# Optimization experiments

Measured on AMD Instinct MI355X. Metric: run time of the kernel, lower is better.

Reference implementation:

```python
import jax, jax.numpy as jnp
import numpy as np

N, M, D = 8192, 8192, 64


def setup_inputs() -> dict:
    key = jax.random.key(0)
    k1, k2 = jax.random.split(key)
    return {
        "x": jax.random.normal(k1, (N, D), dtype=jnp.float32),
        "y": jax.random.normal(k2, (M, D), dtype=jnp.float32),
        "log_lengthscale": jnp.zeros((D,), dtype=jnp.float32),
        "log_outputscale": jnp.zeros((1,), dtype=jnp.float32),
    }


def reference(x, y, log_lengthscale, log_outputscale):
    # ARD RBF: k(x,y) = outputscale * exp(-0.5 * sum_d ((x_d - y_d)/l_d)^2)
    lengthscale = jnp.exp(log_lengthscale)          # [D]
    outputscale = jnp.exp(log_outputscale)          # [1]
    xs = x / lengthscale                            # [N, D]
    ys = y / lengthscale                            # [M, D]
    # ||xs - ys||^2 = ||xs||^2 + ||ys||^2 - 2 xs.ys^T  (GEMM rewrite, same math)
    x2 = jnp.sum(xs * xs, axis=-1)                  # [N]
    y2 = jnp.sum(ys * ys, axis=-1)                  # [M]
    cross = jnp.einsum("nd,md->nm", xs, ys)         # [N, M]
    sq_dist = jnp.maximum(x2[:, None] + y2[None, :] - 2.0 * cross, 0.0)
    return outputscale * jnp.exp(-0.5 * sq_dist)    # [N, M]
```

## Files before the change

kernel.cpp:

```cpp
#include <hip/hip_runtime.h>
#include <hip/hip_bf16.h>

#define NROWS 8192
#define MCOLS 8192
#define DDIM  64

typedef __attribute__((ext_vector_type(8))) short bf16x8;
typedef __attribute__((ext_vector_type(4))) float f32x4;
typedef __attribute__((ext_vector_type(2))) unsigned int u32x2;
typedef __attribute__((ext_vector_type(4))) unsigned int u32x4;

#define WS_NEED (4ull * 1024 * 1024 + 64 * 1024)

__global__ __launch_bounds__(256)
void pack_kernel(const float* __restrict__ x, const float* __restrict__ y,
                 const float* __restrict__ log_l, unsigned char* __restrict__ ws)
{
    const int t = threadIdx.x, lane = t & 63, wid = t >> 6;
    const int sub = lane & 15, lg = lane >> 4;
    const int gb  = blockIdx.x;
    const int isY = gb >> 7;
    const int rb  = ((gb & 127) << 2) | wid;

    const float* __restrict__ src = isY ? y : x;
    bf16x8* __restrict__ Ph = reinterpret_cast<bf16x8*>(ws + (isY ? (2u << 20) : 0u));
    bf16x8* __restrict__ Pl = reinterpret_cast<bf16x8*>(ws + (isY ? (3u << 20) : (1u << 20)));
    float*  __restrict__ nrm = reinterpret_cast<float*>(ws + (4u << 20) + (isY ? (32u << 10) : 0u));

    const int row = rb * 16 + sub;
    float psum = 0.0f;
    #pragma unroll
    for (int kk = 0; kk < 2; ++kk) {
        const int k0 = kk * 32 + lg * 8;
        f32x4 v0 = *reinterpret_cast<const f32x4*>(&src[(size_t)row * DDIM + k0]);
        f32x4 v1 = *reinterpret_cast<const f32x4*>(&src[(size_t)row * DDIM + k0 + 4]);
        f32x4 g0 = *reinterpret_cast<const f32x4*>(&log_l[k0]);
        f32x4 g1 = *reinterpret_cast<const f32x4*>(&log_l[k0 + 4]);
        float s[8];
        #pragma unroll
        for (int j = 0; j < 4; ++j) s[j]     = v0[j] * __expf(-g0[j]);
        #pragma unroll
        for (int j = 0; j < 4; ++j) s[4 + j] = v1[j] * __expf(-g1[j]);
        unsigned int hp[4], lp[4];
        #pragma unroll
        for (int p = 0; p < 4; ++p) {
            float a = s[2 * p], b = s[2 * p + 1];
            psum += a * a + b * b;
            unsigned int ua = __float_as_uint(a), ub = __float_as_uint(b);
            float la = a - __uint_as_float(ua & 0xFFFF0000u);
            float lb = b - __uint_as_float(ub & 0xFFFF0000u);
            hp[p] = (ua >> 16) | (ub & 0xFFFF0000u);
            lp[p] = ((__float_as_uint(la) + 0x8000u) >> 16) |
                    ((__float_as_uint(lb) + 0x8000u) & 0xFFFF0000u);
        }
        const int fi = (rb * 2 + kk) * 64 + lane;
        *reinterpret_cast<u32x4*>(&Ph[fi]) = u32x4{hp[0], hp[1], hp[2], hp[3]};
        *reinterpret_cast<u32x4*>(&Pl[fi]) = u32x4{lp[0], lp[1], lp[2], lp[3]};
    }
    psum += __shfl_xor(psum, 16);
    psum += __shfl_xor(psum, 32);
    if (lg == 0) nrm[row] = psum;
}

__global__ __launch_bounds__(256, 4)
void ard_rbf_main(const unsigned char* __restrict__ ws,
                  const float* __restrict__ log_os, float* __restrict__ out)
{
    const int t = threadIdx.x, lane = t & 63, wid = t >> 6;
    const int sub = lane & 15, lg = lane >> 4;
    const int bx = blockIdx.x;
    const int by = blockIdx.y;
    const int wr = wid >> 1, wc = wid & 1;

    const bf16x8* __restrict__ Xh = reinterpret_cast<const bf16x8*>(ws);
    const bf16x8* __restrict__ Xl = reinterpret_cast<const bf16x8*>(ws + (1u << 20));
    const bf16x8* __restrict__ Yh = reinterpret_cast<const bf16x8*>(ws + (2u << 20));
    const bf16x8* __restrict__ Yl = reinterpret_cast<const bf16x8*>(ws + (3u << 20));
    const float*  __restrict__ x2 = reinterpret_cast<const float*>(ws + (4u << 20));
    const float*  __restrict__ y2 = reinterpret_cast<const float*>(ws + (4u << 20) + (32u << 10));

    const int row0 = by * 128 + wr * 64;
    const int col0 = bx * 64 + wc * 32;
    const int rbA = row0 >> 4, rbB = col0 >> 4;

    f32x4 acc[4][2] = {};
    #pragma unroll
    for (int kk = 0; kk < 2; ++kk) {
        bf16x8 ah[4], al[4];
        #pragma unroll
        for (int m = 0; m < 4; ++m) {
            const int fi = ((rbA + m) * 2 + kk) * 64 + lane;
            ah[m] = Xh[fi];
            al[m] = Xl[fi];
        }
        #pragma unroll
        for (int n = 0; n < 2; ++n) {
            const int fj = ((rbB + n) * 2 + kk) * 64 + lane;
            bf16x8 bh = Yh[fj];
            bf16x8 bl = Yl[fj];
            #pragma unroll
            for (int m = 0; m < 4; ++m) {
                acc[m][n] = __builtin_amdgcn_mfma_f32_16x16x32_bf16(ah[m], bh, acc[m][n], 0, 0, 0);
                acc[m][n] = __builtin_amdgcn_mfma_f32_16x16x32_bf16(al[m], bh, acc[m][n], 0, 0, 0);
                acc[m][n] = __builtin_amdgcn_mfma_f32_16x16x32_bf16(ah[m], bl, acc[m][n], 0, 0, 0);
            }
        }
    }

    const float lnos = log_os[0];
    float y2v[2];
    #pragma unroll
    for (int n = 0; n < 2; ++n) y2v[n] = y2[col0 + n * 16 + sub];

    #pragma unroll
    for (int m = 0; m < 4; ++m) {
        const int rbase = row0 + m * 16 + lg * 4;
        float x2v[4];
        #pragma unroll
        for (int j = 0; j < 4; ++j) x2v[j] = x2[rbase + j];
        #pragma unroll
        for (int n = 0; n < 2; ++n) {
            const size_t g0 = (size_t)rbase * MCOLS + (size_t)(col0 + n * 16 + sub);
            #pragma unroll
            for (int j = 0; j < 4; ++j) {
                float sq = fmaxf(x2v[j] + y2v[n] - 2.0f * acc[m][n][j], 0.0f);
                out[g0 + (size_t)j * MCOLS] = __expf(fmaf(-0.5f, sq, lnos));
            }
        }
    }
}

__global__ __launch_bounds__(512, 4)
void ard_rbf_fallback(const float* __restrict__ x, const float* __restrict__ y,
                      const float* __restrict__ log_l, const float* __restrict__ log_os,
                      float* __restrict__ out)
{
    __shared__ unsigned short Ah[128][DDIM + 8], Al[128][DDIM + 8];
    __shared__ unsigned short Bh[128][DDIM + 8], Bl[128][DDIM + 8];
    __shared__ float x2s[128], y2s[128];
    __shared__ float invl[DDIM];

    const int t = threadIdx.x;
    const int bx = blockIdx.x, by = blockIdx.y;
    const int lane = t & 63, sub = lane & 15, lg = lane >> 4;

    if (t < DDIM) invl[t] = __expf(-log_l[t]);
    __syncthreads();

    #pragma unroll
    for (int ab = 0; ab < 2; ++ab) {
        const float* __restrict__ src = ab ? y : x;
        unsigned short (*Hh)[DDIM + 8] = ab ? Bh : Ah;
        unsigned short (*Hl)[DDIM + 8] = ab ? Bl : Al;
        float* nrm = ab ? y2s : x2s;
        const int tb = (ab ? bx : by) * 128;
        #pragma unroll
        for (int i = 0; i < 4; ++i) {
            const int f = i * 512 + t;
            const int row = f >> 4;
            const int c4 = (f & 15) * 4;
            f32x4 v = *reinterpret_cast<const f32x4*>(&src[(size_t)(tb + row) * DDIM + c4]);
            f32x4 il = *reinterpret_cast<const f32x4*>(&invl[c4]);
            float s0 = v[0] * il[0], s1 = v[1] * il[1], s2 = v[2] * il[2], s3 = v[3] * il[3];
            float psum = s0 * s0 + s1 * s1 + s2 * s2 + s3 * s3;
            unsigned int u0 = __float_as_uint(s0), u1 = __float_as_uint(s1);
            unsigned int u2 = __float_as_uint(s2), u3 = __float_as_uint(s3);
            float l0 = s0 - __uint_as_float(u0 & 0xFFFF0000u);
            float l1 = s1 - __uint_as_float(u1 & 0xFFFF0000u);
            float l2 = s2 - __uint_as_float(u2 & 0xFFFF0000u);
            float l3 = s3 - __uint_as_float(u3 & 0xFFFF0000u);
            unsigned int hp0 = (u0 >> 16) | (u1 & 0xFFFF0000u);
            unsigned int hp1 = (u2 >> 16) | (u3 & 0xFFFF0000u);
            unsigned int lp0 = ((__float_as_uint(l0) + 0x8000u) >> 16) | ((__float_as_uint(l1) + 0x8000u) & 0xFFFF0000u);
            unsigned int lp1 = ((__float_as_uint(l2) + 0x8000u) >> 16) | ((__float_as_uint(l3) + 0x8000u) & 0xFFFF0000u);
            psum += __shfl_xor(psum, 1);
            psum += __shfl_xor(psum, 2);
            psum += __shfl_xor(psum, 4);
            psum += __shfl_xor(psum, 8);
            *reinterpret_cast<u32x2*>(&Hh[row][c4]) = u32x2{hp0, hp1};
            *reinterpret_cast<u32x2*>(&Hl[row][c4]) = u32x2{lp0, lp1};
            if (sub == 0) nrm[row] = psum;
        }
    }
    __syncthreads();

    const int wid = t >> 6;
    const int wr = wid >> 2, wc = wid & 3;
    f32x4 acc[4][2] = {};
    #pragma unroll
    for (int kk = 0; kk < 2; ++kk) {
        const int kb = kk * 32 + lg * 8;
        bf16x8 ah[4], al[4];
        #pragma unroll
        for (int m = 0; m < 4; ++m) {
            const int r = wr * 64 + m * 16 + sub;
            ah[m] = *reinterpret_cast<const bf16x8*>(&Ah[r][kb]);
            al[m] = *reinterpret_cast<const bf16x8*>(&Al[r][kb]);
        }
        #pragma unroll
        for (int n = 0; n < 2; ++n) {
            const int c = wc * 32 + n * 16 + sub;
            bf16x8 bh = *reinterpret_cast<const bf16x8*>(&Bh[c][kb]);
            bf16x8 bl = *reinterpret_cast<const bf16x8*>(&Bl[c][kb]);
            #pragma unroll
            for (int m = 0; m < 4; ++m) {
                acc[m][n] = __builtin_amdgcn_mfma_f32_16x16x32_bf16(ah[m], bh, acc[m][n], 0, 0, 0);
                acc[m][n] = __builtin_amdgcn_mfma_f32_16x16x32_bf16(al[m], bh, acc[m][n], 0, 0, 0);
                acc[m][n] = __builtin_amdgcn_mfma_f32_16x16x32_bf16(ah[m], bl, acc[m][n], 0, 0, 0);
            }
        }
    }
    const float lnos = log_os[0];
    #pragma unroll
    for (int m = 0; m < 4; ++m) {
        const int rl0 = wr * 64 + m * 16 + lg * 4;
        #pragma unroll
        for (int n = 0; n < 2; ++n) {
            const int cl = wc * 32 + n * 16 + sub;
            const float yy2 = y2s[cl];
            const size_t g0 = (size_t)(by * 128 + rl0) * MCOLS + (size_t)(bx * 128 + cl);
            #pragma unroll
            for (int j = 0; j < 4; ++j) {
                float sq = fmaxf(x2s[rl0 + j] + yy2 - 2.0f * acc[m][n][j], 0.0f);
                out[g0 + (size_t)j * MCOLS] = __expf(fmaf(-0.5f, sq, lnos));
            }
        }
    }
}

extern "C" void kernel_launch(void* const* d_in, const int* in_sizes, int n_in,
                              void* d_out, int out_size, void* d_ws, size_t ws_size,
                              hipStream_t stream) {
    const float* x      = (const float*)d_in[0];
    const float* y      = (const float*)d_in[1];
    const float* log_l  = (const float*)d_in[2];
    const float* log_os = (const float*)d_in[3];
    float* out = (float*)d_out;

    if (ws_size >= WS_NEED) {
        pack_kernel<<<256, 256, 0, stream>>>(x, y, log_l, (unsigned char*)d_ws);
        ard_rbf_main<<<dim3(128, 64), 256, 0, stream>>>((const unsigned char*)d_ws, log_os, out);
    } else {
        ard_rbf_fallback<<<dim3(64, 64), 512, 0, stream>>>(x, y, log_l, log_os, out);
    }
}
```

Baseline: 61.06 us.

## Swap MFMA operands for row-contiguous vector stores and swizzle blocks across XCDs

Swaps the MFMA A/B operands so each lane holds four consecutive output columns of one row. That allows 16-byte nontemporal vector stores instead of scalar strided stores. The grid becomes 1D with a block-index swizzle that maps consecutive blocks to different XCD groups, aiming at better L2 locality. The y2 norms are now loaded as float4. The goal is to cut store-transaction overhead on the 256MB output write, which is the dominant cost.

Result: slower. 83.10 us (+36.1%).

```diff
diff --git a/kernel.cpp b/kernel.cpp
--- a/kernel.cpp
+++ b/kernel.cpp
@@ -68,9 +68,13 @@
 {
     const int t = threadIdx.x, lane = t & 63, wid = t >> 6;
     const int sub = lane & 15, lg = lane >> 4;
-    const int bx = blockIdx.x;
-    const int by = blockIdx.y;
-    const int wr = wid >> 1, wc = wid & 1;
+
+    const int bid = (int)blockIdx.x;
+    const int swz = (bid & 7) * 1024 + (bid >> 3);
+    const int by  = swz >> 7;
+    const int bx  = swz & 127;
+    const int wr  = wid >> 1;
+    const int wc  = wid & 1;
 
     const bf16x8* __restrict__ Xh = reinterpret_cast<const bf16x8*>(ws);
     const bf16x8* __restrict__ Xl = reinterpret_cast<const bf16x8*>(ws + (1u << 20));
@@ -79,53 +83,59 @@
     const float*  __restrict__ x2 = reinterpret_cast<const float*>(ws + (4u << 20));
     const float*  __restrict__ y2 = reinterpret_cast<const float*>(ws + (4u << 20) + (32u << 10));
 
-    const int row0 = by * 128 + wr * 64;
-    const int col0 = bx * 64 + wc * 32;
-    const int rbA = row0 >> 4, rbB = col0 >> 4;
+    const int xrb = by * 8 + wr * 4;
+    const int yrb = bx * 4 + wc * 2;
 
     f32x4 acc[4][2] = {};
     #pragma unroll
     for (int kk = 0; kk < 2; ++kk) {
-        bf16x8 ah[4], al[4];
+        bf16x8 yh[2], yl[2], xh[4], xl[4];
+        #pragma unroll
+        for (int n = 0; n < 2; ++n) {
+            const int fj = ((yrb + n) * 2 + kk) * 64 + lane;
+            yh[n] = Yh[fj];
+            yl[n] = Yl[fj];
+        }
         #pragma unroll
         for (int m = 0; m < 4; ++m) {
-            const int fi = ((rbA + m) * 2 + kk) * 64 + lane;
-            ah[m] = Xh[fi];
-            al[m] = Xl[fi];
-        }
-        #pragma unroll
-        for (int n = 0; n < 2; ++n) {
-            const int fj = ((rbB + n) * 2 + kk) * 64 + lane;
-            bf16x8 bh = Yh[fj];
-            bf16x8 bl = Yl[fj];
-            #pragma unroll
-            for (int m = 0; m < 4; ++m) {
-                acc[m][n] = __builtin_amdgcn_mfma_f32_16x16x32_bf16(ah[m], bh, acc[m][n], 0, 0, 0);
-                acc[m][n] = __builtin_amdgcn_mfma_f32_16x16x32_bf16(al[m], bh, acc[m][n], 0, 0, 0);
-                acc[m][n] = __builtin_amdgcn_mfma_f32_16x16x32_bf16(ah[m], bl, acc[m][n], 0, 0, 0);
-            }
-        }
+            const int fi = ((xrb + m) * 2 + kk) * 64 + lane;
+            xh[m] = Xh[fi];
+            xl[m] = Xl[fi];
+        }
+        #pragma unroll
+        for (int m = 0; m < 4; ++m)
+            #pragma unroll
+            for (int n = 0; n < 2; ++n) {
+                acc[m][n] = __builtin_amdgcn_mfma_f32_16x16x32_bf16(yh[n], xh[m], acc[m][n], 0, 0, 0);
+                acc[m][n] = __builtin_amdgcn_mfma_f32_16x16x32_bf16(yl[n], xh[m], acc[m][n], 0, 0, 0);
+                acc[m][n] = __builtin_amdgcn_mfma_f32_16x16x32_bf16(yh[n], xl[m], acc[m][n], 0, 0, 0);
+            }
     }
 
     const float lnos = log_os[0];
-    float y2v[2];
-    #pragma unroll
-    for (int n = 0; n < 2; ++n) y2v[n] = y2[col0 + n * 16 + sub];
+    const int xbase = by * 128 + wr * 64;
+    const int ybase = bx * 64 + wc * 32;
+
+    f32x4 y2q[2];
+    #pragma unroll
+    for (int n = 0; n < 2; ++n)
+        y2q[n] = *reinterpret_cast<const f32x4*>(&y2[ybase + n * 16 + lg * 4]);
 
     #pragma unroll
     for (int m = 0; m < 4; ++m) {
-        const int rbase = row0 + m * 16 + lg * 4;
-        float x2v[4];
-        #pragma unroll
-        for (int j = 0; j < 4; ++j) x2v[j] = x2[rbase + j];
-        #pragma unroll
-        for (int n = 0; n < 2; ++n) {
-            const size_t g0 = (size_t)rbase * MCOLS + (size_t)(col0 + n * 16 + sub);
+        const int xrow = xbase + m * 16 + sub;
+        const float xs = x2[xrow];
+        float* rowp = out + (size_t)xrow * MCOLS;
+        #pragma unroll
+        for (int n = 0; n < 2; ++n) {
+            const int ycol = ybase + n * 16 + lg * 4;
+            f32x4 v;
             #pragma unroll
             for (int j = 0; j < 4; ++j) {
-                float sq = fmaxf(x2v[j] + y2v[n] - 2.0f * acc[m][n][j], 0.0f);
-                out[g0 + (size_t)j * MCOLS] = __expf(fmaf(-0.5f, sq, lnos));
-            }
+                float sq = fmaxf(xs + y2q[n][j] - 2.0f * acc[m][n][j], 0.0f);
+                v[j] = __expf(fmaf(-0.5f, sq, lnos));
+            }
+            __builtin_nontemporal_store(v, reinterpret_cast<f32x4*>(rowp + ycol));
         }
     }
 }
@@ -239,7 +249,7 @@
 
     if (ws_size >= WS_NEED) {
         pack_kernel<<<256, 256, 0, stream>>>(x, y, log_l, (unsigned char*)d_ws);
-        ard_rbf_main<<<dim3(128, 64), 256, 0, stream>>>((const unsigned char*)d_ws, log_os, out);
+        ard_rbf_main<<<8192, 256, 0, stream>>>((const unsigned char*)d_ws, log_os, out);
     } else {
         ard_rbf_fallback<<<dim3(64, 64), 512, 0, stream>>>(x, y, log_l, log_os, out);
     }
```

## Stage MFMA tiles through LDS for 16-byte coalesced output stores

Applied to the files above, without the earlier changes.

Swaps the MFMA operand order so the accumulators come out transposed. Each wave now owns 32 rows by 64 columns, writes its tile to a padded LDS buffer, and reads it back so every lane stores a contiguous float4 of output. Before, each lane wrote scalar floats spread across rows. The goal is fewer, wider global writes for an output-bandwidth-bound kernel (256MB written). The cost is LDS use and an extra shared-memory round trip per tile, which may lower occupancy.

Measured after the change: 63.17 us. 3.5% more time.

```diff
diff --git a/kernel.cpp b/kernel.cpp
--- a/kernel.cpp
+++ b/kernel.cpp
@@ -66,11 +66,12 @@
 void ard_rbf_main(const unsigned char* __restrict__ ws,
                   const float* __restrict__ log_os, float* __restrict__ out)
 {
+    __shared__ float lds[4][32][68];
+
     const int t = threadIdx.x, lane = t & 63, wid = t >> 6;
     const int sub = lane & 15, lg = lane >> 4;
     const int bx = blockIdx.x;
     const int by = blockIdx.y;
-    const int wr = wid >> 1, wc = wid & 1;
 
     const bf16x8* __restrict__ Xh = reinterpret_cast<const bf16x8*>(ws);
     const bf16x8* __restrict__ Xl = reinterpret_cast<const bf16x8*>(ws + (1u << 20));
@@ -79,54 +80,58 @@
     const float*  __restrict__ x2 = reinterpret_cast<const float*>(ws + (4u << 20));
     const float*  __restrict__ y2 = reinterpret_cast<const float*>(ws + (4u << 20) + (32u << 10));
 
-    const int row0 = by * 128 + wr * 64;
-    const int col0 = bx * 64 + wc * 32;
-    const int rbA = row0 >> 4, rbB = col0 >> 4;
-
-    f32x4 acc[4][2] = {};
+    const int xrb = by * 8 + wid * 2;
+    const int yrb = bx * 4;
+
+    f32x4 acc[2][4] = {};
     #pragma unroll
     for (int kk = 0; kk < 2; ++kk) {
-        bf16x8 ah[4], al[4];
-        #pragma unroll
-        for (int m = 0; m < 4; ++m) {
-            const int fi = ((rbA + m) * 2 + kk) * 64 + lane;
-            ah[m] = Xh[fi];
-            al[m] = Xl[fi];
-        }
-        #pragma unroll
-        for (int n = 0; n < 2; ++n) {
-            const int fj = ((rbB + n) * 2 + kk) * 64 + lane;
-            bf16x8 bh = Yh[fj];
-            bf16x8 bl = Yl[fj];
+        bf16x8 xh[2], xl[2], yh[4], yl[4];
+        #pragma unroll
+        for (int a = 0; a < 2; ++a) {
+            const int fi = ((xrb + a) * 2 + kk) * 64 + lane;
+            xh[a] = Xh[fi];
+            xl[a] = Xl[fi];
+        }
+        #pragma unroll
+        for (int b = 0; b < 4; ++b) {
+            const int fj = ((yrb + b) * 2 + kk) * 64 + lane;
+            yh[b] = Yh[fj];
+            yl[b] = Yl[fj];
+        }
+        #pragma unroll
+        for (int a = 0; a < 2; ++a)
             #pragma unroll
-            for (int m = 0; m < 4; ++m) {
-                acc[m][n] = __builtin_amdgcn_mfma_f32_16x16x32_bf16(ah[m], bh, acc[m][n], 0, 0, 0);
-                acc[m][n] = __builtin_amdgcn_mfma_f32_16x16x32_bf16(al[m], bh, acc[m][n], 0, 0, 0);
-                acc[m][n] = __builtin_amdgcn_mfma_f32_16x16x32_bf16(ah[m], bl, acc[m][n], 0, 0, 0);
+            for (int b = 0; b < 4; ++b) {
+                acc[a][b] = __builtin_amdgcn_mfma_f32_16x16x32_bf16(yh[b], xh[a], acc[a][b], 0, 0, 0);
+                acc[a][b] = __builtin_amdgcn_mfma_f32_16x16x32_bf16(yl[b], xh[a], acc[a][b], 0, 0, 0);
+                acc[a][b] = __builtin_amdgcn_mfma_f32_16x16x32_bf16(yh[b], xl[a], acc[a][b], 0, 0, 0);
             }
-        }
-    }
+    }
+
+    #pragma unroll
+    for (int a = 0; a < 2; ++a)
+        #pragma unroll
+        for (int b = 0; b < 4; ++b)
+            *reinterpret_cast<f32x4*>(&lds[wid][a * 16 + sub][b * 16 + lg * 4]) = acc[a][b];
 
     const float lnos = log_os[0];
-    float y2v[2];
-    #pragma unroll
-    for (int n = 0; n < 2; ++n) y2v[n] = y2[col0 + n * 16 + sub];
-
-    #pragma unroll
-    for (int m = 0; m < 4; ++m) {
-        const int rbase = row0 + m * 16 + lg * 4;
-        float x2v[4];
-        #pragma unroll
-        for (int j = 0; j < 4; ++j) x2v[j] = x2[rbase + j];
-        #pragma unroll
-        for (int n = 0; n < 2; ++n) {
-            const size_t g0 = (size_t)rbase * MCOLS + (size_t)(col0 + n * 16 + sub);
-            #pragma unroll
-            for (int j = 0; j < 4; ++j) {
-                float sq = fmaxf(x2v[j] + y2v[n] - 2.0f * acc[m][n][j], 0.0f);
-                out[g0 + (size_t)j * MCOLS] = __expf(fmaf(-0.5f, sq, lnos));
-            }
-        }
+    const int xbase = by * 128 + wid * 32;
+    const int ybase = bx * 64;
+    const f32x4 y2q = *reinterpret_cast<const f32x4*>(&y2[ybase + sub * 4]);
+
+    #pragma unroll
+    for (int r = 0; r < 8; ++r) {
+        const int rloc = r * 4 + lg;
+        f32x4 c = *reinterpret_cast<const f32x4*>(&lds[wid][rloc][sub * 4]);
+        const float xs = x2[xbase + rloc];
+        f32x4 v;
+        #pragma unroll
+        for (int j = 0; j < 4; ++j) {
+            float sq = fmaxf(xs + y2q[j] - 2.0f * c[j], 0.0f);
+            v[j] = __expf(fmaf(-0.5f, sq, lnos));
+        }
+        *reinterpret_cast<f32x4*>(out + (size_t)(xbase + rloc) * MCOLS + ybase + sub * 4) = v;
     }
 }
 
```

## Transpose MFMA tiles through LDS for row-contiguous vectorized output stores

Applied to the files above, without the earlier changes.

The main kernel is reorganized so each block owns 128 output columns and loops over eight 64-row tiles. It swaps the MFMA operand order, stages each wave's accumulators through a padded LDS buffer, and writes 16-byte vectors along contiguous output rows instead of scattered 4-byte stores. The epilogue is folded algebraically into a single exp of cross plus precomputed -0.5*norm terms. This drops the max(0) clamp, so results can slightly exceed outputscale when rounding makes the squared distance negative. The aim is better write coalescing on the 256 MB output stream, at the cost of LDS traffic and repeated Y fragment loads per iteration.

After: 102.1 us. +67.2%, slower.

```diff
diff --git a/kernel.cpp b/kernel.cpp
--- a/kernel.cpp
+++ b/kernel.cpp
@@ -66,11 +66,14 @@
 void ard_rbf_main(const unsigned char* __restrict__ ws,
                   const float* __restrict__ log_os, float* __restrict__ out)
 {
+    __shared__ float tr[4][16][132];
+
     const int t = threadIdx.x, lane = t & 63, wid = t >> 6;
     const int sub = lane & 15, lg = lane >> 4;
+    const int h   = lane >> 5;
+    const int hc  = lane & 31;
     const int bx = blockIdx.x;
-    const int by = blockIdx.y;
-    const int wr = wid >> 1, wc = wid & 1;
+    const int g  = blockIdx.y;
 
     const bf16x8* __restrict__ Xh = reinterpret_cast<const bf16x8*>(ws);
     const bf16x8* __restrict__ Xl = reinterpret_cast<const bf16x8*>(ws + (1u << 20));
@@ -79,53 +82,49 @@
     const float*  __restrict__ x2 = reinterpret_cast<const float*>(ws + (4u << 20));
     const float*  __restrict__ y2 = reinterpret_cast<const float*>(ws + (4u << 20) + (32u << 10));
 
-    const int row0 = by * 128 + wr * 64;
-    const int col0 = bx * 64 + wc * 32;
-    const int rbA = row0 >> 4, rbB = col0 >> 4;
-
-    f32x4 acc[4][2] = {};
-    #pragma unroll
-    for (int kk = 0; kk < 2; ++kk) {
-        bf16x8 ah[4], al[4];
-        #pragma unroll
-        for (int m = 0; m < 4; ++m) {
-            const int fi = ((rbA + m) * 2 + kk) * 64 + lane;
-            ah[m] = Xh[fi];
-            al[m] = Xl[fi];
-        }
-        #pragma unroll
-        for (int n = 0; n < 2; ++n) {
-            const int fj = ((rbB + n) * 2 + kk) * 64 + lane;
-            bf16x8 bh = Yh[fj];
-            bf16x8 bl = Yl[fj];
-            #pragma unroll
-            for (int m = 0; m < 4; ++m) {
-                acc[m][n] = __builtin_amdgcn_mfma_f32_16x16x32_bf16(ah[m], bh, acc[m][n], 0, 0, 0);
-                acc[m][n] = __builtin_amdgcn_mfma_f32_16x16x32_bf16(al[m], bh, acc[m][n], 0, 0, 0);
-                acc[m][n] = __builtin_amdgcn_mfma_f32_16x16x32_bf16(ah[m], bl, acc[m][n], 0, 0, 0);
+    const float lnos = log_os[0];
+    const int cb = bx * 128;
+    const f32x4 y2q = *reinterpret_cast<const f32x4*>(&y2[cb + hc * 4]);
+    f32x4 ny;
+    #pragma unroll
+    for (int j = 0; j < 4; ++j) ny[j] = -0.5f * y2q[j];
+
+    #pragma unroll
+    for (int it = 0; it < 8; ++it) {
+        const int bt = g * 8 + it;
+
+        f32x4 acc[8] = {};
+        #pragma unroll
+        for (int kk = 0; kk < 2; ++kk) {
+            const int fi = ((bt * 4 + wid) * 2 + kk) * 64 + lane;
+            bf16x8 xh = Xh[fi];
+            bf16x8 xl = Xl[fi];
+            #pragma unroll
+            for (int b = 0; b < 8; ++b) {
+                const int fj = ((bx * 8 + b) * 2 + kk) * 64 + lane;
+                bf16x8 yh = Yh[fj];
+                bf16x8 yl = Yl[fj];
+                acc[b] = __builtin_amdgcn_mfma_f32_16x16x32_bf16(yh, xh, acc[b], 0, 0, 0);
+                acc[b] = __builtin_amdgcn_mfma_f32_16x16x32_bf16(yl, xh, acc[b], 0, 0, 0);
+                acc[b] = __builtin_amdgcn_mfma_f32_16x16x32_bf16(yh, xl, acc[b], 0, 0, 0);
             }
         }
-    }
-
-    const float lnos = log_os[0];
-    float y2v[2];
-    #pragma unroll
-    for (int n = 0; n < 2; ++n) y2v[n] = y2[col0 + n * 16 + sub];
-
-    #pragma unroll
-    for (int m = 0; m < 4; ++m) {
-        const int rbase = row0 + m * 16 + lg * 4;
-        float x2v[4];
-        #pragma unroll
-        for (int j = 0; j < 4; ++j) x2v[j] = x2[rbase + j];
-        #pragma unroll
-        for (int n = 0; n < 2; ++n) {
-            const size_t g0 = (size_t)rbase * MCOLS + (size_t)(col0 + n * 16 + sub);
-            #pragma unroll
-            for (int j = 0; j < 4; ++j) {
-                float sq = fmaxf(x2v[j] + y2v[n] - 2.0f * acc[m][n][j], 0.0f);
-                out[g0 + (size_t)j * MCOLS] = __expf(fmaf(-0.5f, sq, lnos));
-            }
+
+        #pragma unroll
+        for (int b = 0; b < 8; ++b)
+            *reinterpret_cast<f32x4*>(&tr[wid][sub][b * 16 + lg * 4]) = acc[b];
+
+        const int xb = bt * 64 + wid * 16;
+        #pragma unroll
+        for (int s = 0; s < 8; ++s) {
+            const int rl = s * 2 + h;
+            f32x4 c = *reinterpret_cast<const f32x4*>(&tr[wid][rl][hc * 4]);
+            const float pre = fmaf(-0.5f, x2[xb + rl], lnos);
+            f32x4 v;
+            #pragma unroll
+            for (int j = 0; j < 4; ++j)
+                v[j] = __expf(c[j] + (pre + ny[j]));
+            *reinterpret_cast<f32x4*>(out + (size_t)(xb + rl) * MCOLS + cb + hc * 4) = v;
         }
     }
 }
@@ -239,7 +238,7 @@
 
     if (ws_size >= WS_NEED) {
         pack_kernel<<<256, 256, 0, stream>>>(x, y, log_l, (unsigned char*)d_ws);
-        ard_rbf_main<<<dim3(128, 64), 256, 0, stream>>>((const unsigned char*)d_ws, log_os, out);
+        ard_rbf_main<<<dim3(64, 16), 256, 0, stream>>>((const unsigned char*)d_ws, log_os, out);
     } else {
         ard_rbf_fallback<<<dim3(64, 64), 512, 0, stream>>>(x, y, log_l, log_os, out);
     }
```
